# Performance work log

Hardware: AMD Instinct MI355X
Metric: run time of the kernel (lower is better)

## Reference

```python
import jax, jax.numpy as jnp
import numpy as np

EPS = 1e-6
B, N, E = 2, 100000, 400000
NODE_DIM, NUM_FEAT = 32, 32
H0, H1 = 128, 64   # state_encoder_hidden_size
D = 64             # gcn_node_dim


def setup_inputs() -> dict:
    key = jax.random.key(0)
    ks = jax.random.split(key, 12)
    def lin(k, fan_in, shape):
        b = 1.0 / np.sqrt(fan_in)
        return jax.random.uniform(k, shape, jnp.float32, -b, b)
    return {
        "numerical": jax.random.normal(ks[0], (B, NUM_FEAT), jnp.float32),
        "node_feature": jax.random.normal(ks[1], (B, N, NODE_DIM), jnp.float32),
        "edge_index": jax.random.randint(ks[2], (B, E, 2), 0, N),
        "edge_mask": jax.random.randint(ks[3], (B, E), 0, 2).astype(bool),
        "stage": jax.random.normal(ks[4], (B, 2), jnp.float32),
        # numerical feature encoder: Linear(32->128) tanh, Linear(128->64) tanh
        "W1": lin(ks[5], NUM_FEAT, (NUM_FEAT, H0)), "b1": lin(ks[6], NUM_FEAT, (H0,)),
        "W2": lin(ks[7], H0, (H0, H1)), "b2": lin(ks[8], H0, (H1,)),
        # node encoder: Linear(32->64) tanh
        "Wn": lin(ks[9], NODE_DIM, (NODE_DIM, D)), "bn": lin(ks[10], NODE_DIM, (D,)),
        # edge_fc: Linear(128->64) tanh
        "We": lin(ks[11], 2 * D, (2 * D, D)),
        "be": lin(jax.random.fold_in(key, 99), 2 * D, (D,)),
    }


def reference(numerical, node_feature, edge_index, edge_mask, stage,
              W1, b1, W2, b2, Wn, bn, We, be):
    # numerical feature encoder
    h_num = jnp.tanh(jnp.tanh(numerical @ W1 + b1) @ W2 + b2)       # [B, H1]
    # node encoder
    h_nodes = jnp.tanh(node_feature @ Wn + bn)                       # [B, N, D]
    # gather node feats to edge endpoints
    h1 = jnp.take_along_axis(h_nodes, edge_index[:, :, 0:1], axis=1)  # [B, E, D]
    h2 = jnp.take_along_axis(h_nodes, edge_index[:, :, 1:2], axis=1)  # [B, E, D]
    # edge_fc applied to [h1,h2] and [h2,h1], averaged. Split We to avoid concat.
    Wa, Wb = We[:D], We[D:]
    e12 = jnp.tanh(h1 @ Wa + h2 @ Wb + be)
    e21 = jnp.tanh(h2 @ Wa + h1 @ Wb + be)
    h_edges = 0.5 * (e12 + e21)                                       # [B, E, D]
    m = edge_mask[:, :, None]
    h_edges = jnp.where(m, h_edges, 0.0)
    # masked mean over edges
    mf = edge_mask.astype(h_edges.dtype)
    h_mean = (h_edges * mf[:, :, None]).sum(axis=1) / mf.sum(axis=1, keepdims=True)
    state_value = jnp.concatenate([h_num, h_mean, stage], axis=-1)    # [B, H1+D+2]
    state_policy = h_edges                                            # [B, E, D]
    return (state_policy, state_value)
```

## Files before the change

### kernel.cpp

```cpp
#include <hip/hip_runtime.h>
#include <hip/hip_bf16.h>

typedef __attribute__((ext_vector_type(4))) float  f32x4;
typedef __attribute__((ext_vector_type(8))) __bf16 bf16x8;

#define NB 2
#define NN 100000
#define NE 400000

__device__ __forceinline__ float tanh_f(float x) {
  float y = __builtin_amdgcn_fmed3f(2.f * x, -40.f, 40.f);
  float e = __expf(y);
  return fmaf(-2.f, __builtin_amdgcn_rcpf(e + 1.f), 1.f);
}

__device__ __forceinline__ float ldf(const void* p, long i, int bf) {
  return bf ? (float)((const __bf16*)p)[i] : ((const float*)p)[i];
}

__global__ __launch_bounds__(256) void k_setup(
    const unsigned int* __restrict__ mw, const unsigned int* __restrict__ nodew,
    const void* __restrict__ numerical, const void* __restrict__ W1,
    const void* __restrict__ b1, const void* __restrict__ W2,
    const void* __restrict__ b2, const void* __restrict__ Wn,
    const void* __restrict__ bn, const void* __restrict__ We,
    int* __restrict__ flags, float* __restrict__ hnum,
    float* __restrict__ sums, float* __restrict__ counts,
    __bf16* __restrict__ packWn, __bf16* __restrict__ packWe,
    float* __restrict__ packBn) {
  __shared__ int badS, goodS, dtS;
  __shared__ float numf[2][32];
  __shared__ float u[2][128];
  const int t = threadIdx.x;
  if (t == 0) { badS = 0; goodS = 0; }
  __syncthreads();
  int my = 0;
  for (int i = t; i < 4096; i += 256) my |= (mw[i] > 1u) ? 1 : 0;
  if (my) atomicOr(&badS, 1);
  int g = 0;
  for (int i = t; i < 4096; i += 256) {
    unsigned lo = nodew[i] & 0xFFFFu;
    unsigned e = (lo >> 7) & 0xFFu;
    g += (lo == 0u || (e >= 100u && e <= 141u)) ? 1 : 0;
  }
  atomicAdd(&goodS, g);
  __syncthreads();
  if (t == 0) {
    flags[0] = badS;
    dtS = (goodS > 2048) ? 1 : 0;
    flags[1] = dtS;
  }
  __syncthreads();
  const int dt = dtS;

  if (t < 128) sums[t] = 0.f;
  if (t < 2) counts[t] = 0.f;
  if (t < 64) numf[t >> 5][t & 31] = ldf(numerical, t, dt);
  __syncthreads();
  {
    const int b = t >> 7, j = t & 127;
    float acc = ldf(b1, j, dt);
#pragma unroll
    for (int k = 0; k < 32; ++k) acc += numf[b][k] * ldf(W1, k * 128 + j, dt);
    u[b][j] = tanh_f(acc);
  }
  __syncthreads();
  if (t < 128) {
    const int b = t >> 6, d = t & 63;
    float acc = ldf(b2, d, dt);
#pragma unroll
    for (int k = 0; k < 128; ++k) acc += u[b][k] * ldf(W2, k * 64 + d, dt);
    hnum[b * 64 + d] = tanh_f(acc);
  }

  if (t < 64) {
    const int m = t & 15, quad = t >> 4;
#pragma unroll
    for (int nt = 0; nt < 4; ++nt) {
      const int c = m + 16 * nt;
#pragma unroll
      for (int j = 0; j < 8; ++j)
        packWn[t * 32 + nt * 8 + j] = (__bf16)ldf(Wn, (quad * 8 + j) * 64 + c, dt);
      packBn[t * 4 + nt] = ldf(bn, c, dt);
    }
#pragma unroll
    for (int f = 0; f < 16; ++f) {
      const int s = f >> 2, nt = f & 3;
      const int n = m + 16 * nt;
#pragma unroll
      for (int j = 0; j < 8; ++j) {
        const int k = s * 32 + quad * 8 + j;
        packWe[t * 128 + f * 8 + j] = (__bf16)ldf(We, (long)k * 64 + n, dt);
      }
    }
  }
}

__global__ __launch_bounds__(256) void k_nodes(
    const void* __restrict__ node, const __bf16* __restrict__ packWn,
    const float* __restrict__ packBn, const int* __restrict__ flags,
    __bf16* __restrict__ hG) {
  const int t = threadIdx.x;
  const int wave = t >> 6, lane = t & 63;
  const int m = lane & 15, quad = lane >> 4;
  const int dt = flags[1];

  bf16x8 wnF[4];
#pragma unroll
  for (int nt = 0; nt < 4; ++nt)
    wnF[nt] = *(const bf16x8*)(packWn + lane * 32 + nt * 8);
  float bnv[4];
#pragma unroll
  for (int nt = 0; nt < 4; ++nt) bnv[nt] = packBn[lane * 4 + nt];

  const long r0 = ((long)blockIdx.x * 4 + wave) * 16;
  bf16x8 aF;
  if (dt) {
    aF = *(const bf16x8*)((const __bf16*)node + (r0 + m) * 32 + quad * 8);
  } else {
    const float* p = (const float*)node + (r0 + m) * 32 + quad * 8;
    f32x4 v0 = *(const f32x4*)p, v1 = *(const f32x4*)(p + 4);
#pragma unroll
    for (int j = 0; j < 4; ++j) { aF[j] = (__bf16)v0[j]; aF[4 + j] = (__bf16)v1[j]; }
  }

  f32x4 acc[4];
#pragma unroll
  for (int nt = 0; nt < 4; ++nt) {
    f32x4 c; c[0] = bnv[nt]; c[1] = bnv[nt]; c[2] = bnv[nt]; c[3] = bnv[nt];
    acc[nt] = c;
  }
#pragma unroll
  for (int nt = 0; nt < 4; ++nt)
    acc[nt] = __builtin_amdgcn_mfma_f32_16x16x32_bf16(aF, wnF[nt], acc[nt], 0, 0, 0);

  __bf16* out = hG + r0 * 64;
#pragma unroll
  for (int nt = 0; nt < 4; ++nt)
#pragma unroll
    for (int r = 0; r < 4; ++r)
      out[(quad * 4 + r) * 64 + m + 16 * nt] = (__bf16)tanh_f(acc[nt][r]);
}

__global__ __launch_bounds__(256) void k_edges(
    const int2* __restrict__ eidx, const void* __restrict__ emask,
    const int* __restrict__ flags, const __bf16* __restrict__ hG,
    const __bf16* __restrict__ packWe, const void* __restrict__ be,
    float* __restrict__ sums, float* __restrict__ counts,
    float* __restrict__ outp) {
  const int nbPerB = (NE + 255) / 256;
  const int b = blockIdx.x / nbPerB;
  const long e0 = (long)(blockIdx.x % nbPerB) * 256;
  const int t = threadIdx.x;
  const int wave = t >> 6, lane = t & 63;
  const int m = lane & 15, quad = lane >> 4;
  const int dt = flags[1], mode = flags[0];

  __shared__ int2 eL[256];
  __shared__ float mL[256];
  __shared__ float red[4][64];
  __shared__ float redc[4];

  {
    const long e = e0 + t;
    const int valid = (e < NE) ? 1 : 0;
    const long ec = valid ? e : (NE - 1);
    eL[t] = eidx[(long)b * NE + ec];
    float mv;
    if (mode) mv = (float)(((const unsigned char*)emask)[(long)b * NE + ec]);
    else      mv = (float)(((const int*)emask)[(long)b * NE + ec]);
    mL[t] = valid ? mv : 0.f;
  }
  __syncthreads();

  bf16x8 weF[16];
#pragma unroll
  for (int f = 0; f < 16; ++f)
    weF[f] = *(const bf16x8*)(packWe + lane * 128 + f * 8);
  float be2[4];
#pragma unroll
  for (int nt = 0; nt < 4; ++nt) be2[nt] = 2.f * ldf(be, m + 16 * nt, dt);

  const __bf16* hb = hG + (long)b * NN * 64;
  float psum[4] = {0.f, 0.f, 0.f, 0.f};

  bf16x8 a0, a1, a2, a3;
  {
    const int2 ij = eL[wave * 64 + m];
    const __bf16* hi = hb + (long)ij.x * 64;
    const __bf16* hj = hb + (long)ij.y * 64;
    a0 = *(const bf16x8*)(hi + quad * 8);
    a1 = *(const bf16x8*)(hi + 32 + quad * 8);
    a2 = *(const bf16x8*)(hj + quad * 8);
    a3 = *(const bf16x8*)(hj + 32 + quad * 8);
  }

#pragma unroll
  for (int it = 0; it < 4; ++it) {
    const int slot = wave * 64 + it * 16;
    const bf16x8 c0 = a0, c1 = a1, c2 = a2, c3 = a3;
    if (it < 3) {
      const int2 ij = eL[slot + 16 + m];
      const __bf16* hi = hb + (long)ij.x * 64;
      const __bf16* hj = hb + (long)ij.y * 64;
      a0 = *(const bf16x8*)(hi + quad * 8);
      a1 = *(const bf16x8*)(hi + 32 + quad * 8);
      a2 = *(const bf16x8*)(hj + quad * 8);
      a3 = *(const bf16x8*)(hj + 32 + quad * 8);
    }

    f32x4 acc12[4], acc21[4];
#pragma unroll
    for (int nt = 0; nt < 4; ++nt) {
      f32x4 z; z[0] = 0.f; z[1] = 0.f; z[2] = 0.f; z[3] = 0.f;
      acc12[nt] = z; acc21[nt] = z;
    }
#pragma unroll
    for (int nt = 0; nt < 4; ++nt) {
      acc12[nt] = __builtin_amdgcn_mfma_f32_16x16x32_bf16(c0, weF[nt], acc12[nt], 0, 0, 0);
      acc21[nt] = __builtin_amdgcn_mfma_f32_16x16x32_bf16(c2, weF[nt], acc21[nt], 0, 0, 0);
    }
#pragma unroll
    for (int nt = 0; nt < 4; ++nt) {
      acc12[nt] = __builtin_amdgcn_mfma_f32_16x16x32_bf16(c1, weF[4 + nt], acc12[nt], 0, 0, 0);
      acc21[nt] = __builtin_amdgcn_mfma_f32_16x16x32_bf16(c3, weF[4 + nt], acc21[nt], 0, 0, 0);
    }
#pragma unroll
    for (int nt = 0; nt < 4; ++nt) {
      acc12[nt] = __builtin_amdgcn_mfma_f32_16x16x32_bf16(c2, weF[8 + nt], acc12[nt], 0, 0, 0);
      acc21[nt] = __builtin_amdgcn_mfma_f32_16x16x32_bf16(c0, weF[8 + nt], acc21[nt], 0, 0, 0);
    }
#pragma unroll
    for (int nt = 0; nt < 4; ++nt) {
      acc12[nt] = __builtin_amdgcn_mfma_f32_16x16x32_bf16(c3, weF[12 + nt], acc12[nt], 0, 0, 0);
      acc21[nt] = __builtin_amdgcn_mfma_f32_16x16x32_bf16(c1, weF[12 + nt], acc21[nt], 0, 0, 0);
    }

    const long egbase = e0 + slot;
#pragma unroll
    for (int r = 0; r < 4; ++r) {
      const long e = egbase + quad * 4 + r;
      if (e >= NE) continue;
      const float mvr = mL[slot + quad * 4 + r];
      float* op = outp + ((long)b * NE + e) * 64 + m;
#pragma unroll
      for (int nt = 0; nt < 4; ++nt) {
        float x12 = __builtin_amdgcn_fmed3f(
            fmaf(acc12[nt][r], 2.f, be2[nt]), -40.f, 40.f);
        float x21 = __builtin_amdgcn_fmed3f(
            fmaf(acc21[nt][r], 2.f, be2[nt]), -40.f, 40.f);
        const float p12 = __builtin_amdgcn_rcpf(__expf(x12) + 1.f);
        const float p21 = __builtin_amdgcn_rcpf(__expf(x21) + 1.f);
        const float v = mvr * (1.f - p12 - p21);
        psum[nt] += v;
        __builtin_nontemporal_store(v, op + 16 * nt);
      }
    }
  }

#pragma unroll
  for (int nt = 0; nt < 4; ++nt) {
    psum[nt] += __shfl_xor(psum[nt], 16);
    psum[nt] += __shfl_xor(psum[nt], 32);
  }
  if (quad == 0) {
#pragma unroll
    for (int nt = 0; nt < 4; ++nt) red[wave][m + 16 * nt] = psum[nt];
  }
  float pc = mL[t];
#pragma unroll
  for (int d = 1; d < 64; d <<= 1) pc += __shfl_xor(pc, d);
  if (lane == 0) redc[wave] = pc;
  __syncthreads();
  if (t < 64) {
    const float s = red[0][t] + red[1][t] + red[2][t] + red[3][t];
    atomicAdd(&sums[b * 64 + t], s);
  }
  if (t == 0) atomicAdd(&counts[b], redc[0] + redc[1] + redc[2] + redc[3]);
}

__global__ __launch_bounds__(512) void k_final(
    const float* __restrict__ hnum, const float* __restrict__ sums,
    const float* __restrict__ counts, const void* __restrict__ stage,
    const int* __restrict__ flags, float* __restrict__ out) {
  const int t = threadIdx.x;
  const int dt = flags[1];
  if (t < 260) {
    const int b = t / 130, c = t % 130;
    float v;
    if (c < 64) v = hnum[b * 64 + c];
    else if (c < 128) v = sums[b * 64 + (c - 64)] / counts[b];
    else v = ldf(stage, b * 2 + (c - 128), dt);
    out[(long)NB * NE * 64 + (long)b * 130 + c] = v;
  }
}

extern "C" void kernel_launch(void* const* d_in, const int* in_sizes, int n_in,
                              void* d_out, int out_size, void* d_ws, size_t ws_size,
                              hipStream_t stream) {
  const void* numerical = d_in[0];
  const void* node      = d_in[1];
  const int2* eidx      = (const int2*)d_in[2];
  const void* emask     = d_in[3];
  const void* stage     = d_in[4];
  const void* W1 = d_in[5];
  const void* b1 = d_in[6];
  const void* W2 = d_in[7];
  const void* b2 = d_in[8];
  const void* Wn = d_in[9];
  const void* bn = d_in[10];
  const void* We = d_in[11];
  const void* be = d_in[12];

  char* ws = (char*)d_ws;
  int*    flags  = (int*)ws;
  float*  sums   = (float*)(ws + 256);
  float*  counts = (float*)(ws + 1024);
  float*  hnum   = (float*)(ws + 1280);
  float*  packBn = (float*)(ws + 2048);
  __bf16* packWn = (__bf16*)(ws + 4096);
  __bf16* packWe = (__bf16*)(ws + 8192);
  __bf16* hG     = (__bf16*)(ws + 32768);
  float*  outp   = (float*)d_out;

  k_setup<<<1, 256, 0, stream>>>((const unsigned int*)emask, (const unsigned int*)node,
                                 numerical, W1, b1, W2, b2, Wn, bn, We,
                                 flags, hnum, sums, counts, packWn, packWe, packBn);
  k_nodes<<<(NB * NN) / 64, 256, 0, stream>>>(node, packWn, packBn, flags, hG);
  k_edges<<<NB * ((NE + 255) / 256), 256, 0, stream>>>(eidx, emask, flags, hG, packWe, be,
                                                       sums, counts, outp);
  k_final<<<1, 512, 0, stream>>>(hnum, sums, counts, stage, flags, outp);
}
```

Measured before the change: 395.9 us.

## Stage edge weights in LDS, double edges per block, deepen gather prefetch

The packed edge_fc weight fragments move from per-lane registers (16 bf16x8 per lane) into shared memory, re-laid out so each wave reads conflict-free vectors per k-slice. Each block now handles 512 edges, eight 16-edge iterations per wave, with a three-deep rotating gather buffer prefetching two tiles ahead. Launch bounds request four blocks per CU. The goal is to free registers for occupancy and hide the latency of the random node gathers. In exchange it adds LDS traffic inside the MFMA loop and uses more shared memory per block.

```diff
diff --git a/kernel.cpp b/kernel.cpp
--- a/kernel.cpp
+++ b/kernel.cpp
@@ -7,6 +7,7 @@
 #define NB 2
 #define NN 100000
 #define NE 400000
+#define EPB 512
 
 __device__ __forceinline__ float tanh_f(float x) {
   float y = __builtin_amdgcn_fmed3f(2.f * x, -40.f, 40.f);
@@ -90,7 +91,7 @@
 #pragma unroll
       for (int j = 0; j < 8; ++j) {
         const int k = s * 32 + quad * 8 + j;
-        packWe[t * 128 + f * 8 + j] = (__bf16)ldf(We, (long)k * 64 + n, dt);
+        packWe[(f * 64 + t) * 8 + j] = (__bf16)ldf(We, (long)k * 64 + n, dt);
       }
     }
   }
@@ -142,71 +143,74 @@
       out[(quad * 4 + r) * 64 + m + 16 * nt] = (__bf16)tanh_f(acc[nt][r]);
 }
 
-__global__ __launch_bounds__(256) void k_edges(
+__global__ __launch_bounds__(256, 4) void k_edges(
     const int2* __restrict__ eidx, const void* __restrict__ emask,
     const int* __restrict__ flags, const __bf16* __restrict__ hG,
     const __bf16* __restrict__ packWe, const void* __restrict__ be,
     float* __restrict__ sums, float* __restrict__ counts,
     float* __restrict__ outp) {
-  const int nbPerB = (NE + 255) / 256;
+  const int nbPerB = (NE + EPB - 1) / EPB;
   const int b = blockIdx.x / nbPerB;
-  const long e0 = (long)(blockIdx.x % nbPerB) * 256;
+  const long e0 = (long)(blockIdx.x % nbPerB) * EPB;
   const int t = threadIdx.x;
   const int wave = t >> 6, lane = t & 63;
   const int m = lane & 15, quad = lane >> 4;
   const int dt = flags[1], mode = flags[0];
 
-  __shared__ int2 eL[256];
-  __shared__ float mL[256];
+  __shared__ __bf16 weL[64 * 128];
+  __shared__ int2 eL[EPB];
+  __shared__ float mL[EPB];
   __shared__ float red[4][64];
   __shared__ float redc[4];
 
   {
-    const long e = e0 + t;
+    const bf16x8* src = (const bf16x8*)packWe;
+    bf16x8* dst = (bf16x8*)weL;
+#pragma unroll
+    for (int u = 0; u < 4; ++u) dst[t + 256 * u] = src[t + 256 * u];
+  }
+#pragma unroll
+  for (int u = 0; u < 2; ++u) {
+    const int idx = t + 256 * u;
+    const long e = e0 + idx;
     const int valid = (e < NE) ? 1 : 0;
     const long ec = valid ? e : (NE - 1);
-    eL[t] = eidx[(long)b * NE + ec];
+    eL[idx] = eidx[(long)b * NE + ec];
     float mv;
     if (mode) mv = (float)(((const unsigned char*)emask)[(long)b * NE + ec]);
     else      mv = (float)(((const int*)emask)[(long)b * NE + ec]);
-    mL[t] = valid ? mv : 0.f;
-  }
-  __syncthreads();
-
-  bf16x8 weF[16];
-#pragma unroll
-  for (int f = 0; f < 16; ++f)
-    weF[f] = *(const bf16x8*)(packWe + lane * 128 + f * 8);
+    mL[idx] = valid ? mv : 0.f;
+  }
+  __syncthreads();
+
   float be2[4];
 #pragma unroll
   for (int nt = 0; nt < 4; ++nt) be2[nt] = 2.f * ldf(be, m + 16 * nt, dt);
 
   const __bf16* hb = hG + (long)b * NN * 64;
+  const int wslot = wave * 128;
   float psum[4] = {0.f, 0.f, 0.f, 0.f};
 
-  bf16x8 a0, a1, a2, a3;
-  {
-    const int2 ij = eL[wave * 64 + m];
-    const __bf16* hi = hb + (long)ij.x * 64;
-    const __bf16* hj = hb + (long)ij.y * 64;
-    a0 = *(const bf16x8*)(hi + quad * 8);
-    a1 = *(const bf16x8*)(hi + 32 + quad * 8);
-    a2 = *(const bf16x8*)(hj + quad * 8);
-    a3 = *(const bf16x8*)(hj + 32 + quad * 8);
-  }
-
-#pragma unroll
-  for (int it = 0; it < 4; ++it) {
-    const int slot = wave * 64 + it * 16;
-    const bf16x8 c0 = a0, c1 = a1, c2 = a2, c3 = a3;
-    if (it < 3) {
-      const int2 ij = eL[slot + 16 + m];
-      const __bf16* hi = hb + (long)ij.x * 64;
-      const __bf16* hj = hb + (long)ij.y * 64;
-      a0 = *(const bf16x8*)(hi + quad * 8);
-      a1 = *(const bf16x8*)(hi + 32 + quad * 8);
-      a2 = *(const bf16x8*)(hj + quad * 8);
-      a3 = *(const bf16x8*)(hj + 32 + quad * 8);
+  bf16x8 A[3][4];
+#define GATHER(SET, TT)                                             \
+  {                                                                 \
+    const int2 ij = eL[wslot + (TT) * 16 + m];                      \
+    const __bf16* hi = hb + (long)ij.x * 64;                        \
+    const __bf16* hj = hb + (long)ij.y * 64;                        \
+    A[SET][0] = *(const bf16x8*)(hi + quad * 8);                    \
+    A[SET][1] = *(const bf16x8*)(hi + 32 + quad * 8);               \
+    A[SET][2] = *(const bf16x8*)(hj + quad * 8);                    \
+    A[SET][3] = *(const bf16x8*)(hj + 32 + quad * 8);               \
+  }
+  GATHER(0, 0)
+  GATHER(1, 1)
+
+#pragma unroll
+  for (int it = 0; it < 8; ++it) {
+    const int cb = it % 3;
+    if (it + 2 < 8) {
+      const int pb = (it + 2) % 3;
+      GATHER(pb, it + 2)
     }
 
     f32x4 acc12[4], acc21[4];
@@ -216,32 +220,26 @@
       acc12[nt] = z; acc21[nt] = z;
     }
 #pragma unroll
-    for (int nt = 0; nt < 4; ++nt) {
-      acc12[nt] = __builtin_amdgcn_mfma_f32_16x16x32_bf16(c0, weF[nt], acc12[nt], 0, 0, 0);
-      acc21[nt] = __builtin_amdgcn_mfma_f32_16x16x32_bf16(c2, weF[nt], acc21[nt], 0, 0, 0);
-    }
-#pragma unroll
-    for (int nt = 0; nt < 4; ++nt) {
-      acc12[nt] = __builtin_amdgcn_mfma_f32_16x16x32_bf16(c1, weF[4 + nt], acc12[nt], 0, 0, 0);
-      acc21[nt] = __builtin_amdgcn_mfma_f32_16x16x32_bf16(c3, weF[4 + nt], acc21[nt], 0, 0, 0);
-    }
-#pragma unroll
-    for (int nt = 0; nt < 4; ++nt) {
-      acc12[nt] = __builtin_amdgcn_mfma_f32_16x16x32_bf16(c2, weF[8 + nt], acc12[nt], 0, 0, 0);
-      acc21[nt] = __builtin_amdgcn_mfma_f32_16x16x32_bf16(c0, weF[8 + nt], acc21[nt], 0, 0, 0);
-    }
-#pragma unroll
-    for (int nt = 0; nt < 4; ++nt) {
-      acc12[nt] = __builtin_amdgcn_mfma_f32_16x16x32_bf16(c3, weF[12 + nt], acc12[nt], 0, 0, 0);
-      acc21[nt] = __builtin_amdgcn_mfma_f32_16x16x32_bf16(c1, weF[12 + nt], acc21[nt], 0, 0, 0);
-    }
-
-    const long egbase = e0 + slot;
+    for (int s = 0; s < 4; ++s) {
+      bf16x8 w[4];
+#pragma unroll
+      for (int nt = 0; nt < 4; ++nt)
+        w[nt] = *(const bf16x8*)(weL + ((4 * s + nt) * 64 + lane) * 8);
+      const bf16x8 a12 = A[cb][s];
+      const bf16x8 a21 = A[cb][s ^ 2];
+#pragma unroll
+      for (int nt = 0; nt < 4; ++nt) {
+        acc12[nt] = __builtin_amdgcn_mfma_f32_16x16x32_bf16(a12, w[nt], acc12[nt], 0, 0, 0);
+        acc21[nt] = __builtin_amdgcn_mfma_f32_16x16x32_bf16(a21, w[nt], acc21[nt], 0, 0, 0);
+      }
+    }
+
+    const long egbase = e0 + wslot + it * 16;
 #pragma unroll
     for (int r = 0; r < 4; ++r) {
       const long e = egbase + quad * 4 + r;
       if (e >= NE) continue;
-      const float mvr = mL[slot + quad * 4 + r];
+      const float mvr = mL[wslot + it * 16 + quad * 4 + r];
       float* op = outp + ((long)b * NE + e) * 64 + m;
 #pragma unroll
       for (int nt = 0; nt < 4; ++nt) {
@@ -257,6 +255,7 @@
       }
     }
   }
+#undef GATHER
 
 #pragma unroll
   for (int nt = 0; nt < 4; ++nt) {
@@ -267,7 +266,7 @@
 #pragma unroll
     for (int nt = 0; nt < 4; ++nt) red[wave][m + 16 * nt] = psum[nt];
   }
-  float pc = mL[t];
+  float pc = mL[t] + mL[t + 256];
 #pragma unroll
   for (int d = 1; d < 64; d <<= 1) pc += __shfl_xor(pc, d);
   if (lane == 0) redc[wave] = pc;
@@ -327,7 +326,7 @@
                                  numerical, W1, b1, W2, b2, Wn, bn, We,
                                  flags, hnum, sums, counts, packWn, packWe, packBn);
   k_nodes<<<(NB * NN) / 64, 256, 0, stream>>>(node, packWn, packBn, flags, hG);
-  k_edges<<<NB * ((NE + 255) / 256), 256, 0, stream>>>(eidx, emask, flags, hG, packWe, be,
-                                                       sums, counts, outp);
+  k_edges<<<NB * ((NE + EPB - 1) / EPB), 256, 0, stream>>>(eidx, emask, flags, hG, packWe, be,
+                                                           sums, counts, outp);
   k_final<<<1, 512, 0, stream>>>(hnum, sums, counts, stage, flags, outp);
 }
```

After: 443.9 us. +12.1%, slower.
